# Kernel optimization log

Hardware: AMD Instinct MI355X
Metric: run time of the kernel (lower is better)

Reference implementation:

```python
import jax, jax.numpy as jnp
import numpy as np

B, F, H, S, K, L, C = 128, 8192, 8192, 4, 32, 3, 100  # batch, encoded feats, hidden, segments, synapses/seg, hidden layers, classes


def setup_inputs() -> dict:
    key = jax.random.key(0)
    k1, k2, k3, k4, k5, k6 = jax.random.split(key, 6)
    # binary encoded input activations (thermometer-coded tabular features)
    x = jax.random.randint(k1, (B, F), 0, 2).astype(jnp.float32)
    # sign weights in {-1,+1} for each synapse of each segment of each neuron
    signs0 = jnp.where(jax.random.bernoulli(k2, 0.5, (S, H, K)), 1.0, -1.0).astype(jnp.float32)
    signsH = jnp.where(jax.random.bernoulli(k3, 0.5, (L - 1, S, H, K)), 1.0, -1.0).astype(jnp.float32)
    # synapse source indices (irregular connectivity)
    idx0 = jax.random.randint(k4, (S, H, K), 0, F, dtype=jnp.int32)
    idxH = jax.random.randint(k5, (L - 1, S, H, K), 0, H, dtype=jnp.int32)
    # per-layer output connection matrices [L, H, C]
    wout = jax.random.normal(k6, (L, H, C), dtype=jnp.float32) * 0.02
    return {"x": x, "signs0": signs0, "signsH": signsH, "wout": wout,
            "idx0": idx0, "idxH": idxH, "threshold": 8}


def _segment_layer(a, idx, signs, threshold):
    # a: [B, P] prev activations; idx/signs: [S, H, K]
    g = a[:, idx]                                  # [B, S, H, K] irregular gather
    z = jnp.einsum('bshk,shk->bsh', g, signs)      # per-segment summed input
    fired = jnp.any(z >= threshold, axis=1)        # OR over segments -> [B, H]
    return fired.astype(a.dtype)


def reference(x, signs0, signsH, wout, idx0, idxH, threshold):
    thr = jnp.float32(threshold)
    a = _segment_layer(x, idx0, signs0, thr)       # hidden layer 0
    acts = [a]
    for l in range(idxH.shape[0]):                 # remaining hidden layers (fixed small L)
        a = _segment_layer(a, idxH[l], signsH[l], thr)
        acts.append(a)
    # sum class votes from every hidden layer's output connection matrix
    out = jnp.einsum('lbh,lhc->bc', jnp.stack(acts, 0), wout)  # [B, C]
    return out
```

## Files before the change

kernel.cpp:

```cpp
#include <hip/hip_runtime.h>
#include <stdint.h>

#define B 128
#define F 8192
#define H 8192
#define S 4
#define K 32
#define L 3
#define C 100

__global__ void pack_x_kernel(const float* __restrict__ x, uint32_t* __restrict__ xP,
                              float* __restrict__ out) {
    const int zi = blockIdx.x * 128 + threadIdx.x;
    if (zi < B * C) out[zi] = 0.0f;

    const int b = threadIdx.x;
    const int wv = threadIdx.x >> 6;
    const int f0 = blockIdx.x * 32;
    const float4* xr = (const float4*)(x + (size_t)b * F + f0);
    for (int j = 0; j < 8; ++j) {
        const float4 v = xr[j];
        const uint64_t m0 = __ballot(v.x > 0.5f);
        const uint64_t m1 = __ballot(v.y > 0.5f);
        const uint64_t m2 = __ballot(v.z > 0.5f);
        const uint64_t m3 = __ballot(v.w > 0.5f);
        if ((threadIdx.x & 63) == 0) {
            const int f = f0 + 4 * j;
            uint32_t* lo = xP + (size_t)(2 * wv) * F;
            uint32_t* hi = xP + (size_t)(2 * wv + 1) * F;
            lo[f + 0] = (uint32_t)m0;  hi[f + 0] = (uint32_t)(m0 >> 32);
            lo[f + 1] = (uint32_t)m1;  hi[f + 1] = (uint32_t)(m1 >> 32);
            lo[f + 2] = (uint32_t)m2;  hi[f + 2] = (uint32_t)(m2 >> 32);
            lo[f + 3] = (uint32_t)m3;  hi[f + 3] = (uint32_t)(m3 >> 32);
        }
    }
}

__device__ __forceinline__ int load_threshold(const int* p) {
    int v = *p;
    if (v >= (1 << 23)) v = (int)__int_as_float(v);
    return v;
}

#define ISG_STRIDE 40

__global__ void layer_kernel(const uint32_t* __restrict__ prevP,
                             const int* __restrict__ idx,
                             const float* __restrict__ signs,
                             uint32_t* __restrict__ outP,
                             const int* __restrict__ thrp) {
    __shared__ uint32_t tab[H];
    __shared__ uint32_t isg[S * 64 * ISG_STRIDE];
    __shared__ uint32_t fbuf[256];
    const int tid  = threadIdx.x;
    const int lane = tid & 63;
    const int sw   = tid >> 6;
    const int w    = blockIdx.x & 3;
    const int hg   = blockIdx.x >> 2;
    const int h    = hg * 64 + lane;
    const int thr  = load_threshold(thrp);

    {
        const int4* src = (const int4*)(prevP + (size_t)w * H);
        int4* dst = (int4*)tab;
#pragma unroll
        for (int i = 0; i < 8; ++i)
            dst[i * 256 + tid] = src[i * 256 + tid];
    }
    {
        const int hrow = tid >> 2;
        const int k0   = (tid & 3) * 8;
#pragma unroll
        for (int s = 0; s < S; ++s) {
            const int4*   ib = (const int4*)(idx   + ((size_t)s * H + hg * 64) * K);
            const float4* sb = (const float4*)(signs + ((size_t)s * H + hg * 64) * K);
            const int4   ia = ib[2 * tid],  ic = ib[2 * tid + 1];
            const float4 sa = sb[2 * tid],  sc = sb[2 * tid + 1];
            uint4* dst = (uint4*)(isg + s * (64 * ISG_STRIDE) + hrow * ISG_STRIDE + k0);
            uint4 p0, p1;
            p0.x = (uint32_t)ia.x | ((uint32_t)__float_as_int(sa.x) & 0x80000000u);
            p0.y = (uint32_t)ia.y | ((uint32_t)__float_as_int(sa.y) & 0x80000000u);
            p0.z = (uint32_t)ia.z | ((uint32_t)__float_as_int(sa.z) & 0x80000000u);
            p0.w = (uint32_t)ia.w | ((uint32_t)__float_as_int(sa.w) & 0x80000000u);
            p1.x = (uint32_t)ic.x | ((uint32_t)__float_as_int(sc.x) & 0x80000000u);
            p1.y = (uint32_t)ic.y | ((uint32_t)__float_as_int(sc.y) & 0x80000000u);
            p1.z = (uint32_t)ic.z | ((uint32_t)__float_as_int(sc.z) & 0x80000000u);
            p1.w = (uint32_t)ic.w | ((uint32_t)__float_as_int(sc.w) & 0x80000000u);
            dst[0] = p0;
            dst[1] = p1;
        }
    }
    __syncthreads();

    uint32_t A[6] = {0, 0, 0, 0, 0, 0};
    uint32_t P[6] = {0, 0, 0, 0, 0, 0};
    const uint4* row4 = (const uint4*)(isg + sw * (64 * ISG_STRIDE) + lane * ISG_STRIDE);
#pragma unroll
    for (int c = 0; c < 4; ++c) {
        const uint4 r0 = row4[2 * c];
        const uint4 r1 = row4[2 * c + 1];
        const uint32_t iv[8] = {r0.x, r0.y, r0.z, r0.w, r1.x, r1.y, r1.z, r1.w};
        uint32_t a[8];
#pragma unroll
        for (int j = 0; j < 8; ++j) a[j] = tab[iv[j] & 0xFFFFu];
#pragma unroll
        for (int j = 0; j < 8; ++j) {
            const uint32_t pm = ~(uint32_t)((int32_t)iv[j] >> 31);
            uint32_t cc = a[j];
#pragma unroll
            for (int i = 0; i < 6; ++i) { const uint32_t t = A[i]; A[i] = t ^ cc; cc = t & cc; }
            cc = a[j] & pm;
#pragma unroll
            for (int i = 0; i < 6; ++i) { const uint32_t t = P[i]; P[i] = t ^ cc; cc = t & cc; }
        }
    }

    uint32_t Y[7];
    {
        uint32_t c = 0;
#pragma unroll
        for (int i = 0; i < 7; ++i) {
            const uint32_t ai = (i < 6) ? A[i] : 0u;
            const uint32_t bm = ((thr >> i) & 1) ? 0xFFFFFFFFu : 0u;
            const uint32_t t  = ai ^ bm;
            Y[i] = t ^ c;
            c = (ai & bm) | (t & c);
        }
    }
    uint32_t bw = 0;
#pragma unroll
    for (int i = 0; i < 7; ++i) {
        const uint32_t xx = (i >= 1) ? P[i - 1] : 0u;
        const uint32_t d  = xx ^ Y[i];
        bw = ((~xx) & Y[i]) | ((~d) & bw);
    }
    const uint32_t fired = ~bw;

    fbuf[sw * 64 + lane] = fired;
    __syncthreads();
    if (sw == 0) {
        const uint32_t f = fbuf[lane] | fbuf[64 + lane] |
                           fbuf[128 + lane] | fbuf[192 + lane];
        outP[(size_t)w * H + h] = f;
    }
}

#define NHC 32
#define HCH (H / NHC)

__global__ void final_kernel(const uint32_t* __restrict__ actP,
                             const float* __restrict__ wout,
                             float* __restrict__ out) {
    const int lane = threadIdx.x & 63;
    const int wid  = threadIdx.x >> 6;
    const int hc   = blockIdx.x & (NHC - 1);
    const int bg   = blockIdx.x / NHC;
    const int b    = bg * 4 + wid;
    const int w32  = b >> 5;
    const int bit  = b & 31;

    float acc0 = 0.0f, acc1 = 0.0f;
    const int c1 = 64 + lane;
    const bool c1v = (c1 < C);

    for (int l = 0; l < L; ++l) {
        const uint32_t* aT = actP + ((size_t)l * 4 + w32) * H;
        const float* wl = wout + (size_t)l * H * C;
        for (int r = 0; r < HCH / 64; ++r) {
            const int hbase = hc * HCH + r * 64;
            const uint32_t m = aT[hbase + lane];
            uint64_t hm = __ballot((m >> bit) & 1u);
            while (hm) {
                const int slot = __ffsll((unsigned long long)hm) - 1;
                hm &= hm - 1;
                const float* wr = wl + (size_t)(hbase + slot) * C;
                acc0 += wr[lane];
                if (c1v) acc1 += wr[c1];
            }
        }
    }
    atomicAdd(&out[b * C + lane], acc0);
    if (c1v) atomicAdd(&out[b * C + c1], acc1);
}

extern "C" void kernel_launch(void* const* d_in, const int* in_sizes, int n_in,
                              void* d_out, int out_size, void* d_ws, size_t ws_size,
                              hipStream_t stream) {
    const float* x      = (const float*)d_in[0];
    const float* signs0 = (const float*)d_in[1];
    const float* signsH = (const float*)d_in[2];
    const float* wout   = (const float*)d_in[3];
    const int*   idx0   = (const int*)d_in[4];
    const int*   idxH   = (const int*)d_in[5];
    const int*   thr    = (const int*)d_in[6];
    float* out = (float*)d_out;

    uint32_t* xP   = (uint32_t*)d_ws;
    uint32_t* actP = xP + (size_t)4 * F;

    pack_x_kernel<<<F / 32, 128, 0, stream>>>(x, xP, out);

    layer_kernel<<<512, 256, 0, stream>>>(xP, idx0, signs0, actP, thr);
    layer_kernel<<<512, 256, 0, stream>>>(actP, idxH, signsH,
                                          actP + (size_t)4 * H, thr);
    layer_kernel<<<512, 256, 0, stream>>>(actP + (size_t)4 * H,
                                          idxH + (size_t)S * H * K,
                                          signsH + (size_t)S * H * K,
                                          actP + (size_t)8 * H, thr);

    final_kernel<<<32 * NHC, 256, 0, stream>>>(actP, wout, out);
}
```

Before: 123.2 us.

## Widen pack grid, use async LDS loads, 16-bit index packing, paired final gathers

Several changes at once. The input pack kernel now uses 1024 blocks of 8 features each instead of 256 blocks of 32, for more parallelism. The layer kernel stages the activation table with global_load_lds direct-to-LDS loads, and packs synapse index plus sign into 16-bit entries to halve the shared staging footprint and its reads. The final kernel processes two set bits per iteration so two weight-row loads are in flight together. The 13-bit index mask assumes H and F are at most 8192, and the tab/isg layout and LDS load offsets must line up with the per-wave addressing.

Result: no change. 123.3 us (+0.1%).

```diff
diff --git a/kernel.cpp b/kernel.cpp
--- a/kernel.cpp
+++ b/kernel.cpp
@@ -16,9 +16,10 @@
 
     const int b = threadIdx.x;
     const int wv = threadIdx.x >> 6;
-    const int f0 = blockIdx.x * 32;
+    const int f0 = blockIdx.x * 8;
     const float4* xr = (const float4*)(x + (size_t)b * F + f0);
-    for (int j = 0; j < 8; ++j) {
+#pragma unroll
+    for (int j = 0; j < 2; ++j) {
         const float4 v = xr[j];
         const uint64_t m0 = __ballot(v.x > 0.5f);
         const uint64_t m1 = __ballot(v.y > 0.5f);
@@ -42,7 +43,13 @@
     return v;
 }
 
-#define ISG_STRIDE 40
+__device__ __forceinline__ uint32_t pack2(int i0, float s0, int i1, float s1) {
+    const uint32_t a = (uint32_t)i0 | (((uint32_t)__float_as_int(s0) & 0x80000000u) >> 16);
+    const uint32_t b = (uint32_t)i1 | (((uint32_t)__float_as_int(s1) & 0x80000000u) >> 16);
+    return a | (b << 16);
+}
+
+#define ISG_ST 40
 
 __global__ void layer_kernel(const uint32_t* __restrict__ prevP,
                              const int* __restrict__ idx,
@@ -50,7 +57,7 @@
                              uint32_t* __restrict__ outP,
                              const int* __restrict__ thrp) {
     __shared__ uint32_t tab[H];
-    __shared__ uint32_t isg[S * 64 * ISG_STRIDE];
+    __shared__ uint16_t isg[S * 64 * ISG_ST];
     __shared__ uint32_t fbuf[256];
     const int tid  = threadIdx.x;
     const int lane = tid & 63;
@@ -61,11 +68,15 @@
     const int thr  = load_threshold(thrp);
 
     {
-        const int4* src = (const int4*)(prevP + (size_t)w * H);
-        int4* dst = (int4*)tab;
-#pragma unroll
-        for (int i = 0; i < 8; ++i)
-            dst[i * 256 + tid] = src[i * 256 + tid];
+        const uint32_t* src = prevP + (size_t)w * H;
+#pragma unroll
+        for (int i = 0; i < 8; ++i) {
+            const int off = (sw * 8 + i) * 256;
+            __builtin_amdgcn_global_load_lds(
+                (const __attribute__((address_space(1))) uint32_t*)(src + off + lane * 4),
+                (__attribute__((address_space(3))) uint32_t*)(tab + off),
+                16, 0, 0);
+        }
     }
     {
         const int hrow = tid >> 2;
@@ -76,36 +87,37 @@
             const float4* sb = (const float4*)(signs + ((size_t)s * H + hg * 64) * K);
             const int4   ia = ib[2 * tid],  ic = ib[2 * tid + 1];
             const float4 sa = sb[2 * tid],  sc = sb[2 * tid + 1];
-            uint4* dst = (uint4*)(isg + s * (64 * ISG_STRIDE) + hrow * ISG_STRIDE + k0);
-            uint4 p0, p1;
-            p0.x = (uint32_t)ia.x | ((uint32_t)__float_as_int(sa.x) & 0x80000000u);
-            p0.y = (uint32_t)ia.y | ((uint32_t)__float_as_int(sa.y) & 0x80000000u);
-            p0.z = (uint32_t)ia.z | ((uint32_t)__float_as_int(sa.z) & 0x80000000u);
-            p0.w = (uint32_t)ia.w | ((uint32_t)__float_as_int(sa.w) & 0x80000000u);
-            p1.x = (uint32_t)ic.x | ((uint32_t)__float_as_int(sc.x) & 0x80000000u);
-            p1.y = (uint32_t)ic.y | ((uint32_t)__float_as_int(sc.y) & 0x80000000u);
-            p1.z = (uint32_t)ic.z | ((uint32_t)__float_as_int(sc.z) & 0x80000000u);
-            p1.w = (uint32_t)ic.w | ((uint32_t)__float_as_int(sc.w) & 0x80000000u);
-            dst[0] = p0;
-            dst[1] = p1;
+            uint4 pv;
+            pv.x = pack2(ia.x, sa.x, ia.y, sa.y);
+            pv.y = pack2(ia.z, sa.z, ia.w, sa.w);
+            pv.z = pack2(ic.x, sc.x, ic.y, sc.y);
+            pv.w = pack2(ic.z, sc.z, ic.w, sc.w);
+            *(uint4*)(&isg[s * (64 * ISG_ST) + hrow * ISG_ST + k0]) = pv;
         }
     }
     __syncthreads();
 
     uint32_t A[6] = {0, 0, 0, 0, 0, 0};
     uint32_t P[6] = {0, 0, 0, 0, 0, 0};
-    const uint4* row4 = (const uint4*)(isg + sw * (64 * ISG_STRIDE) + lane * ISG_STRIDE);
-#pragma unroll
-    for (int c = 0; c < 4; ++c) {
-        const uint4 r0 = row4[2 * c];
-        const uint4 r1 = row4[2 * c + 1];
-        const uint32_t iv[8] = {r0.x, r0.y, r0.z, r0.w, r1.x, r1.y, r1.z, r1.w};
+    const uint4* row4 = (const uint4*)(&isg[sw * (64 * ISG_ST) + lane * ISG_ST]);
+#pragma unroll
+    for (int r = 0; r < 4; ++r) {
+        const uint4 q = row4[r];
+        const uint32_t vv[4] = {q.x, q.y, q.z, q.w};
+        uint32_t ik[8], nm[8];
+#pragma unroll
+        for (int j = 0; j < 4; ++j) {
+            ik[2 * j]     = vv[j] & 0x1FFFu;
+            nm[2 * j]     = (uint32_t)((int32_t)(vv[j] << 16) >> 31);
+            ik[2 * j + 1] = (vv[j] >> 16) & 0x1FFFu;
+            nm[2 * j + 1] = (uint32_t)((int32_t)vv[j] >> 31);
+        }
         uint32_t a[8];
 #pragma unroll
-        for (int j = 0; j < 8; ++j) a[j] = tab[iv[j] & 0xFFFFu];
+        for (int j = 0; j < 8; ++j) a[j] = tab[ik[j]];
 #pragma unroll
         for (int j = 0; j < 8; ++j) {
-            const uint32_t pm = ~(uint32_t)((int32_t)iv[j] >> 31);
+            const uint32_t pm = ~nm[j];
             uint32_t cc = a[j];
 #pragma unroll
             for (int i = 0; i < 6; ++i) { const uint32_t t = A[i]; A[i] = t ^ cc; cc = t & cc; }
@@ -171,11 +183,23 @@
             const uint32_t m = aT[hbase + lane];
             uint64_t hm = __ballot((m >> bit) & 1u);
             while (hm) {
-                const int slot = __ffsll((unsigned long long)hm) - 1;
+                const int s0 = __ffsll((unsigned long long)hm) - 1;
                 hm &= hm - 1;
-                const float* wr = wl + (size_t)(hbase + slot) * C;
-                acc0 += wr[lane];
-                if (c1v) acc1 += wr[c1];
+                const float* wr0 = wl + (size_t)(hbase + s0) * C;
+                if (hm) {
+                    const int s1 = __ffsll((unsigned long long)hm) - 1;
+                    hm &= hm - 1;
+                    const float* wr1 = wl + (size_t)(hbase + s1) * C;
+                    const float a0 = wr0[lane];
+                    const float a1 = wr1[lane];
+                    const float b0 = c1v ? wr0[c1] : 0.0f;
+                    const float b1 = c1v ? wr1[c1] : 0.0f;
+                    acc0 += a0 + a1;
+                    acc1 += b0 + b1;
+                } else {
+                    acc0 += wr0[lane];
+                    if (c1v) acc1 += wr0[c1];
+                }
             }
         }
     }
@@ -198,7 +222,7 @@
     uint32_t* xP   = (uint32_t*)d_ws;
     uint32_t* actP = xP + (size_t)4 * F;
 
-    pack_x_kernel<<<F / 32, 128, 0, stream>>>(x, xP, out);
+    pack_x_kernel<<<1024, 128, 0, stream>>>(x, xP, out);
 
     layer_kernel<<<512, 256, 0, stream>>>(xP, idx0, signs0, actP, thr);
     layer_kernel<<<512, 256, 0, stream>>>(actP, idxH, signsH,
```
